# Kernel tuning notes

Hardware: AMD Instinct MI355X
Metric: run time of the kernel (lower is better)

The kernel has to match this reference:

```python
import jax, jax.numpy as jnp
import numpy as np

B, T, C, FREQ = 32, 512, 22, 192
HID = 128


def setup_inputs() -> dict:
    key = jax.random.key(0)
    k1, k2, k3, k4, k5, k6 = jax.random.split(key, 6)
    x = jax.random.normal(k1, (B, T, C, FREQ), dtype=jnp.float32)
    A = jax.random.uniform(k2, (B, T, C, C), dtype=jnp.float32)
    # Linear weights (torch layout: [out, in]); scaled like torch default init
    W0 = jax.random.normal(k3, (HID, FREQ), dtype=jnp.float32) / np.sqrt(FREQ)
    b0 = jax.random.normal(k4, (HID,), dtype=jnp.float32) * 0.01
    W1 = jax.random.normal(k5, (HID, HID), dtype=jnp.float32) / np.sqrt(HID)
    b1 = jax.random.normal(k6, (HID,), dtype=jnp.float32) * 0.01
    return {"x": x, "A": A, "W0": W0, "b0": b0, "W1": W1, "b1": b1}


def reference(x, A, W0, b0, W1, b1):
    # Vectorized over B and T simultaneously (original python-loops over t).
    # Layer i: xt = relu(Linear(bmm(A_t, xt)))
    h = x  # [B,T,C,Freq]
    for W, b in ((W0, b0), (W1, b1)):
        h = jnp.einsum('btij,btjf->btif', A, h)          # adjacency mix over nodes
        h = jax.nn.relu(jnp.einsum('btcf,hf->btch', h, W) + b)  # Linear + ReLU
    # stack over t is implicit; mean over node dim C -> [B,T,HID]
    return h.mean(axis=2)
```

## Files before the change

kernel.cpp:

```cpp
#include <hip/hip_runtime.h>

#define CC 22
#define FF 192
#define HH 128
#define NBT (32 * 512)

typedef __attribute__((ext_vector_type(8))) __bf16 bf16x8;
typedef __attribute__((ext_vector_type(8))) short s16x8;
typedef __attribute__((ext_vector_type(4))) float f32x4;

__device__ __forceinline__ float bf2f(unsigned short u) {
    union { unsigned int i; float f; } v;
    v.i = ((unsigned int)u) << 16;
    return v.f;
}

__device__ __forceinline__ unsigned short f2bf(float f) {
    union { float f; unsigned int i; } v;
    v.f = f;
    return (unsigned short)((v.i + 0x7fffu + ((v.i >> 16) & 1u)) >> 16);
}

__device__ __forceinline__ void split2(float v, unsigned short& h, unsigned short& l) {
    h = f2bf(v);
    float r = v - bf2f(h);
    l = f2bf(r);
}

__device__ __forceinline__ bf16x8 bzero8() {
    s16x8 z = {0, 0, 0, 0, 0, 0, 0, 0};
    return __builtin_bit_cast(bf16x8, z);
}

__global__ void detect_dtype(const unsigned short* __restrict__ A,
                             int* __restrict__ flag) {
    if (blockIdx.x == 0 && threadIdx.x == 0) {
        int ok = 1;
        for (int i = 0; i < 64; ++i) {
            float v = bf2f(A[i]);
            if (!(v >= 0.0f && v <= 1.0001f)) ok = 0;
        }
        *flag = ok;
    }
}

#define WS0H 0
#define WS0L 24576
#define WS1H 49152
#define WS1L 65536

__global__ void convert_weights(const float* __restrict__ W0g,
                                const float* __restrict__ W1g,
                                unsigned short* __restrict__ wsW,
                                const int* __restrict__ flag) {
    if (*flag) return;
    const int i = blockIdx.x * 256 + threadIdx.x;
    if (i < HH * FF) {
        unsigned short h, l;
        split2(W0g[i], h, l);
        wsW[WS0H + i] = h;
        wsW[WS0L + i] = l;
    } else {
        const int j = i - HH * FF;
        if (j < HH * HH) {
            unsigned short h, l;
            split2(W1g[j], h, l);
            wsW[WS1H + j] = h;
            wsW[WS1L + j] = l;
        }
    }
}

__device__ void run_block_f32(
    const float* __restrict__ xg, const float* __restrict__ Ag,
    const float* __restrict__ W0g, const float* __restrict__ b0g,
    const float* __restrict__ W1g, const float* __restrict__ b1g,
    float* __restrict__ outg, int bt, int tid,
    float* sA, float* sX, float* sH1, float* sH2, float* sRed)
{
    const float* Ap = Ag + (size_t)bt * (CC * CC);
    for (int i = tid; i < CC * CC; i += 256) sA[i] = Ap[i];
    const float4* xp = (const float4*)(xg + (size_t)bt * (CC * FF));
    for (int i = tid; i < CC * FF / 4; i += 256) ((float4*)sX)[i] = xp[i];
    __syncthreads();

    for (int idx4 = tid; idx4 < CC * FF / 4; idx4 += 256) {
        const int c  = idx4 / (FF / 4);
        const int fq = idx4 - c * (FF / 4);
        float4 acc = make_float4(0.f, 0.f, 0.f, 0.f);
        #pragma unroll
        for (int j = 0; j < CC; ++j) {
            const float  a  = sA[c * CC + j];
            const float4 xv = *(const float4*)&sX[j * FF + 4 * fq];
            acc.x += a * xv.x; acc.y += a * xv.y;
            acc.z += a * xv.z; acc.w += a * xv.w;
        }
        ((float4*)sH1)[idx4] = acc;
    }
    __syncthreads();

    const int h  = tid & 127;
    const int ty = tid >> 7;

    {
        float acc[11];
        const float bb = b0g[h];
        #pragma unroll
        for (int i = 0; i < 11; ++i) acc[i] = bb;
        #pragma unroll 4
        for (int fq = 0; fq < FF / 4; ++fq) {
            float4 u = ((const float4*)(W0g + h * FF))[fq];
            #pragma unroll
            for (int i = 0; i < 11; ++i) {
                const float4 xv = *(const float4*)&sH1[(2 * i + ty) * FF + 4 * fq];
                acc[i] = fmaf(xv.x, u.x, fmaf(xv.y, u.y, fmaf(xv.z, u.z, fmaf(xv.w, u.w, acc[i]))));
            }
        }
        #pragma unroll
        for (int i = 0; i < 11; ++i)
            sH2[(2 * i + ty) * HH + h] = fmaxf(acc[i], 0.f);
    }
    __syncthreads();

    float* sH3 = sX;
    for (int idx4 = tid; idx4 < CC * HH / 4; idx4 += 256) {
        const int c  = idx4 / (HH / 4);
        const int kq = idx4 - c * (HH / 4);
        float4 acc = make_float4(0.f, 0.f, 0.f, 0.f);
        #pragma unroll
        for (int j = 0; j < CC; ++j) {
            const float  a  = sA[c * CC + j];
            const float4 xv = *(const float4*)&sH2[j * HH + 4 * kq];
            acc.x += a * xv.x; acc.y += a * xv.y;
            acc.z += a * xv.z; acc.w += a * xv.w;
        }
        ((float4*)sH3)[idx4] = acc;
    }
    __syncthreads();

    {
        float acc[11];
        const float bb = b1g[h];
        #pragma unroll
        for (int i = 0; i < 11; ++i) acc[i] = bb;
        #pragma unroll 4
        for (int kq = 0; kq < HH / 4; ++kq) {
            float4 u = ((const float4*)(W1g + h * HH))[kq];
            #pragma unroll
            for (int i = 0; i < 11; ++i) {
                const float4 xv = *(const float4*)&sH3[(2 * i + ty) * HH + 4 * kq];
                acc[i] = fmaf(xv.x, u.x, fmaf(xv.y, u.y, fmaf(xv.z, u.z, fmaf(xv.w, u.w, acc[i]))));
            }
        }
        float s = 0.f;
        #pragma unroll
        for (int i = 0; i < 11; ++i) s += fmaxf(acc[i], 0.f);
        sRed[ty * HH + h] = s;
    }
    __syncthreads();

    if (ty == 0) {
        const float m = (sRed[h] + sRed[HH + h]) * (1.0f / 22.0f);
        outg[(size_t)bt * HH + h] = m;
    }
}

__device__ void run_block_split(
    const float* __restrict__ xg, const float* __restrict__ Ag,
    const float* __restrict__ b0g, const float* __restrict__ b1g,
    const unsigned short* __restrict__ wsW,
    float* __restrict__ outg, int bt, int tid, char* smem)
{
    unsigned short* sxh   = (unsigned short*)smem;
    unsigned short* sxl   = (unsigned short*)(smem + 8800);
    unsigned short* sAh   = (unsigned short*)(smem + 17600);
    unsigned short* sAl   = (unsigned short*)(smem + 20160);
    unsigned short* syTh  = (unsigned short*)(smem + 22720);
    unsigned short* syTl  = (unsigned short*)(smem + 32960);
    unsigned short* sh2Th = (unsigned short*)(smem + 43200);
    unsigned short* sh2Tl = (unsigned short*)(smem + 53440);
    unsigned short* sh3h  = (unsigned short*)smem;
    unsigned short* sh3l  = (unsigned short*)(smem + 8704);

    const unsigned short* W0h = wsW + WS0H;
    const unsigned short* W0l = wsW + WS0L;
    const unsigned short* W1h = wsW + WS1H;
    const unsigned short* W1l = wsW + WS1L;

    {
        const float4* xp4 = (const float4*)(xg + (size_t)bt * (CC * FF));
        for (int idx = tid; idx < CC * (FF / 4); idx += 256) {
            const int c = idx / (FF / 4);
            const int q = idx - c * (FF / 4);
            const float4 v = xp4[idx];
            ushort4 h4, l4;
            split2(v.x, h4.x, l4.x);
            split2(v.y, h4.y, l4.y);
            split2(v.z, h4.z, l4.z);
            split2(v.w, h4.w, l4.w);
            *(ushort4*)&sxh[c * 200 + 4 * q] = h4;
            *(ushort4*)&sxl[c * 200 + 4 * q] = l4;
        }
        const float* Ap = Ag + (size_t)bt * (CC * CC);
        for (int idx = tid; idx < 32 * 40; idx += 256) {
            const int r = idx / 40;
            const int c = idx - r * 40;
            unsigned short h = 0, l = 0;
            if (r < CC && c < CC) split2(Ap[r * CC + c], h, l);
            sAh[idx] = h;
            sAl[idx] = l;
        }
    }
    __syncthreads();

    const int lane = tid & 63;
    const int wid  = tid >> 6;
    const int lr   = lane & 15;
    const int lk   = lane >> 4;
    const int hb   = wid * 32;

    const f32x4 vzero = {0.f, 0.f, 0.f, 0.f};

    {
        f32x4 acc[2][2];
        #pragma unroll
        for (int mt = 0; mt < 2; ++mt)
            #pragma unroll
            for (int nt = 0; nt < 2; ++nt) acc[mt][nt] = vzero;

        #pragma unroll
        for (int ks = 0; ks < 6; ++ks) {
            bf16x8 xfh[2], xfl[2];
            #pragma unroll
            for (int mt = 0; mt < 2; ++mt) {
                const int row = mt * 16 + lr;
                const int rr  = (row < CC) ? row : 0;
                const int off = rr * 200 + ks * 32 + lk * 8;
                bf16x8 fh = *(const bf16x8*)(sxh + off);
                bf16x8 fl = *(const bf16x8*)(sxl + off);
                if (row >= CC) { fh = bzero8(); fl = bzero8(); }
                xfh[mt] = fh; xfl[mt] = fl;
            }
            bf16x8 wfh[2], wfl[2];
            #pragma unroll
            for (int nt = 0; nt < 2; ++nt) {
                const int hcol = hb + nt * 16 + lr;
                const int off  = hcol * FF + ks * 32 + lk * 8;
                wfh[nt] = *(const bf16x8*)(W0h + off);
                wfl[nt] = *(const bf16x8*)(W0l + off);
            }
            #pragma unroll
            for (int mt = 0; mt < 2; ++mt)
                #pragma unroll
                for (int nt = 0; nt < 2; ++nt) {
                    acc[mt][nt] = __builtin_amdgcn_mfma_f32_16x16x32_bf16(xfh[mt], wfh[nt], acc[mt][nt], 0, 0, 0);
                    acc[mt][nt] = __builtin_amdgcn_mfma_f32_16x16x32_bf16(xfl[mt], wfh[nt], acc[mt][nt], 0, 0, 0);
                    acc[mt][nt] = __builtin_amdgcn_mfma_f32_16x16x32_bf16(xfh[mt], wfl[nt], acc[mt][nt], 0, 0, 0);
                }
        }
        #pragma unroll
        for (int mt = 0; mt < 2; ++mt)
            #pragma unroll
            for (int nt = 0; nt < 2; ++nt) {
                const int hcol = hb + nt * 16 + lr;
                ushort4 h4, l4;
                split2(acc[mt][nt][0], h4.x, l4.x);
                split2(acc[mt][nt][1], h4.y, l4.y);
                split2(acc[mt][nt][2], h4.z, l4.z);
                split2(acc[mt][nt][3], h4.w, l4.w);
                *(ushort4*)&syTh[hcol * 40 + mt * 16 + lk * 4] = h4;
                *(ushort4*)&syTl[hcol * 40 + mt * 16 + lk * 4] = l4;
            }
    }
    __syncthreads();

    bf16x8 Afh[2], Afl[2];
    #pragma unroll
    for (int mt = 0; mt < 2; ++mt) {
        const int off = (mt * 16 + lr) * 40 + lk * 8;
        Afh[mt] = *(const bf16x8*)(sAh + off);
        Afl[mt] = *(const bf16x8*)(sAl + off);
    }

    {
        f32x4 acc[2][2];
        #pragma unroll
        for (int nt = 0; nt < 2; ++nt) {
            const float b = b0g[hb + nt * 16 + lr];
            const f32x4 bv = {b, b, b, b};
            acc[0][nt] = bv;
            acc[1][nt] = bv;
        }
        bf16x8 yfh[2], yfl[2];
        #pragma unroll
        for (int nt = 0; nt < 2; ++nt) {
            const int off = (hb + nt * 16 + lr) * 40 + lk * 8;
            yfh[nt] = *(const bf16x8*)(syTh + off);
            yfl[nt] = *(const bf16x8*)(syTl + off);
        }
        #pragma unroll
        for (int mt = 0; mt < 2; ++mt)
            #pragma unroll
            for (int nt = 0; nt < 2; ++nt) {
                acc[mt][nt] = __builtin_amdgcn_mfma_f32_16x16x32_bf16(Afh[mt], yfh[nt], acc[mt][nt], 0, 0, 0);
                acc[mt][nt] = __builtin_amdgcn_mfma_f32_16x16x32_bf16(Afl[mt], yfh[nt], acc[mt][nt], 0, 0, 0);
                acc[mt][nt] = __builtin_amdgcn_mfma_f32_16x16x32_bf16(Afh[mt], yfl[nt], acc[mt][nt], 0, 0, 0);
            }
        #pragma unroll
        for (int mt = 0; mt < 2; ++mt)
            #pragma unroll
            for (int nt = 0; nt < 2; ++nt) {
                const int hcol = hb + nt * 16 + lr;
                ushort4 h4, l4;
                split2(fmaxf(acc[mt][nt][0], 0.f), h4.x, l4.x);
                split2(fmaxf(acc[mt][nt][1], 0.f), h4.y, l4.y);
                split2(fmaxf(acc[mt][nt][2], 0.f), h4.z, l4.z);
                split2(fmaxf(acc[mt][nt][3], 0.f), h4.w, l4.w);
                *(ushort4*)&sh2Th[hcol * 40 + mt * 16 + lk * 4] = h4;
                *(ushort4*)&sh2Tl[hcol * 40 + mt * 16 + lk * 4] = l4;
            }
    }
    __syncthreads();

    {
        f32x4 acc[2][2];
        #pragma unroll
        for (int mt = 0; mt < 2; ++mt)
            #pragma unroll
            for (int nt = 0; nt < 2; ++nt) acc[mt][nt] = vzero;

        bf16x8 gfh[2], gfl[2];
        #pragma unroll
        for (int nt = 0; nt < 2; ++nt) {
            const int off = (hb + nt * 16 + lr) * 40 + lk * 8;
            gfh[nt] = *(const bf16x8*)(sh2Th + off);
            gfl[nt] = *(const bf16x8*)(sh2Tl + off);
        }
        #pragma unroll
        for (int mt = 0; mt < 2; ++mt)
            #pragma unroll
            for (int nt = 0; nt < 2; ++nt) {
                acc[mt][nt] = __builtin_amdgcn_mfma_f32_16x16x32_bf16(Afh[mt], gfh[nt], acc[mt][nt], 0, 0, 0);
                acc[mt][nt] = __builtin_amdgcn_mfma_f32_16x16x32_bf16(Afl[mt], gfh[nt], acc[mt][nt], 0, 0, 0);
                acc[mt][nt] = __builtin_amdgcn_mfma_f32_16x16x32_bf16(Afh[mt], gfl[nt], acc[mt][nt], 0, 0, 0);
            }
        __syncthreads();
        #pragma unroll
        for (int mt = 0; mt < 2; ++mt)
            #pragma unroll
            for (int nt = 0; nt < 2; ++nt) {
                const int col = hb + nt * 16 + lr;
                #pragma unroll
                for (int r = 0; r < 4; ++r) {
                    const int row = mt * 16 + lk * 4 + r;
                    unsigned short h, l;
                    split2(acc[mt][nt][r], h, l);
                    sh3h[row * 136 + col] = h;
                    sh3l[row * 136 + col] = l;
                }
            }
    }
    __syncthreads();

    {
        f32x4 acc[2][2];
        #pragma unroll
        for (int mt = 0; mt < 2; ++mt) {
            const float4 bv = *(const float4*)(b1g + hb + mt * 16 + lk * 4);
            const f32x4 bb = {bv.x, bv.y, bv.z, bv.w};
            acc[mt][0] = bb;
            acc[mt][1] = bb;
        }
        #pragma unroll
        for (int ks = 0; ks < 4; ++ks) {
            bf16x8 wfh[2], wfl[2], hfh[2], hfl[2];
            #pragma unroll
            for (int mt = 0; mt < 2; ++mt) {
                const int o   = hb + mt * 16 + lr;
                const int off = o * HH + ks * 32 + lk * 8;
                wfh[mt] = *(const bf16x8*)(W1h + off);
                wfl[mt] = *(const bf16x8*)(W1l + off);
            }
            #pragma unroll
            for (int ct = 0; ct < 2; ++ct) {
                const int off = (ct * 16 + lr) * 136 + ks * 32 + lk * 8;
                hfh[ct] = *(const bf16x8*)(sh3h + off);
                hfl[ct] = *(const bf16x8*)(sh3l + off);
            }
            #pragma unroll
            for (int mt = 0; mt < 2; ++mt)
                #pragma unroll
                for (int ct = 0; ct < 2; ++ct) {
                    acc[mt][ct] = __builtin_amdgcn_mfma_f32_16x16x32_bf16(wfh[mt], hfh[ct], acc[mt][ct], 0, 0, 0);
                    acc[mt][ct] = __builtin_amdgcn_mfma_f32_16x16x32_bf16(wfl[mt], hfh[ct], acc[mt][ct], 0, 0, 0);
                    acc[mt][ct] = __builtin_amdgcn_mfma_f32_16x16x32_bf16(wfh[mt], hfl[ct], acc[mt][ct], 0, 0, 0);
                }
        }
        float s[2][4];
        #pragma unroll
        for (int mt = 0; mt < 2; ++mt)
            #pragma unroll
            for (int r = 0; r < 4; ++r) {
                float v = fmaxf(acc[mt][0][r], 0.f);
                if (lr < CC - 16) v += fmaxf(acc[mt][1][r], 0.f);
                s[mt][r] = v;
            }
        #pragma unroll
        for (int m = 1; m < 16; m <<= 1)
            #pragma unroll
            for (int mt = 0; mt < 2; ++mt)
                #pragma unroll
                for (int r = 0; r < 4; ++r)
                    s[mt][r] += __shfl_xor(s[mt][r], m);

        if (lr == 0) {
            const float inv = 1.0f / 22.0f;
            #pragma unroll
            for (int mt = 0; mt < 2; ++mt) {
                float4 o4;
                o4.x = s[mt][0] * inv;
                o4.y = s[mt][1] * inv;
                o4.z = s[mt][2] * inv;
                o4.w = s[mt][3] * inv;
                *(float4*)(outg + (size_t)bt * HH + hb + mt * 16 + lk * 4) = o4;
            }
        }
    }
}

__device__ void run_block_bf16(
    const unsigned short* __restrict__ xg, const unsigned short* __restrict__ Ag,
    const unsigned short* __restrict__ W0g, const unsigned short* __restrict__ b0g,
    const unsigned short* __restrict__ W1g, const unsigned short* __restrict__ b1g,
    unsigned short* __restrict__ outg, int bt, int tid, char* smem)
{
    unsigned short* sXT  = (unsigned short*)smem;
    unsigned short* sAm  = (unsigned short*)(smem + 15360);
    unsigned short* sH1  = (unsigned short*)(smem + 17920);
    unsigned short* sH2T = (unsigned short*)(smem + 30720);
    unsigned short* sH3  = (unsigned short*)(smem + 40960);

    const unsigned short* xp = xg + (size_t)bt * (CC * FF);
    const unsigned short* Ap = Ag + (size_t)bt * (CC * CC);

    for (int id = tid; id < 32 * 40; id += 256) {
        const int r = id / 40;
        const int c = id - r * 40;
        sAm[id] = (r < CC && c < CC) ? Ap[r * CC + c] : (unsigned short)0;
    }
    for (int id = tid; id < FF * 9; id += 256) {
        const int f = id / 9;
        const int q = id - f * 9;
        ((unsigned int*)sXT)[f * 20 + 11 + q] = 0u;
    }
    for (int id = tid; id < 24 * CC; id += 256) {
        const int fb = id / CC;
        const int j  = id - fb * CC;
        const uint4 v = *(const uint4*)(xp + j * FF + fb * 8);
        unsigned short* d = sXT + (fb * 8) * 40 + j;
        d[0 * 40] = (unsigned short)(v.x & 0xffffu);
        d[1 * 40] = (unsigned short)(v.x >> 16);
        d[2 * 40] = (unsigned short)(v.y & 0xffffu);
        d[3 * 40] = (unsigned short)(v.y >> 16);
        d[4 * 40] = (unsigned short)(v.z & 0xffffu);
        d[5 * 40] = (unsigned short)(v.z >> 16);
        d[6 * 40] = (unsigned short)(v.w & 0xffffu);
        d[7 * 40] = (unsigned short)(v.w >> 16);
    }
    __syncthreads();

    const int lane = tid & 63;
    const int wid  = tid >> 6;
    const int lr   = lane & 15;
    const int lk   = lane >> 4;
    const f32x4 vzero = {0.f, 0.f, 0.f, 0.f};

    {
        f32x4 acc[3][2];
        #pragma unroll
        for (int i = 0; i < 3; ++i)
            #pragma unroll
            for (int j = 0; j < 2; ++j) acc[i][j] = vzero;
        bf16x8 xa[3], ab[2];
        #pragma unroll
        for (int i = 0; i < 3; ++i)
            xa[i] = *(const bf16x8*)(sXT + ((3 * wid + i) * 16 + lr) * 40 + lk * 8);
        #pragma unroll
        for (int j = 0; j < 2; ++j)
            ab[j] = *(const bf16x8*)(sAm + (j * 16 + lr) * 40 + lk * 8);
        #pragma unroll
        for (int i = 0; i < 3; ++i)
            #pragma unroll
            for (int j = 0; j < 2; ++j)
                acc[i][j] = __builtin_amdgcn_mfma_f32_16x16x32_bf16(xa[i], ab[j], acc[i][j], 0, 0, 0);
        #pragma unroll
        for (int i = 0; i < 3; ++i) {
            const int fbase = (3 * wid + i) * 16 + lk * 4;
            #pragma unroll
            for (int j = 0; j < 2; ++j) {
                const int c = j * 16 + lr;
                ushort4 st;
                st.x = f2bf(acc[i][j][0]);
                st.y = f2bf(acc[i][j][1]);
                st.z = f2bf(acc[i][j][2]);
                st.w = f2bf(acc[i][j][3]);
                *(ushort4*)(sH1 + c * 200 + fbase) = st;
            }
        }
    }
    __syncthreads();

    {
        f32x4 acc[2][2];
        #pragma unroll
        for (int nt = 0; nt < 2; ++nt) {
            const float bv = bf2f(b0g[(2 * wid + nt) * 16 + lr]);
            f32x4 bvv = {bv, bv, bv, bv};
            acc[0][nt] = bvv;
            acc[1][nt] = bvv;
        }
        #pragma unroll
        for (int ks = 0; ks < 6; ++ks) {
            bf16x8 af[2], bfr[2];
            #pragma unroll
            for (int mt = 0; mt < 2; ++mt)
                af[mt] = *(const bf16x8*)(sH1 + (mt * 16 + lr) * 200 + ks * 32 + lk * 8);
            #pragma unroll
            for (int nt = 0; nt < 2; ++nt)
                bfr[nt] = *(const bf16x8*)(W0g + ((size_t)((2 * wid + nt) * 16 + lr)) * FF + ks * 32 + lk * 8);
            #pragma unroll
            for (int mt = 0; mt < 2; ++mt)
                #pragma unroll
                for (int nt = 0; nt < 2; ++nt)
                    acc[mt][nt] = __builtin_amdgcn_mfma_f32_16x16x32_bf16(af[mt], bfr[nt], acc[mt][nt], 0, 0, 0);
        }
        #pragma unroll
        for (int mt = 0; mt < 2; ++mt) {
            const int cbase = mt * 16 + lk * 4;
            #pragma unroll
            for (int nt = 0; nt < 2; ++nt) {
                const int hcol = (2 * wid + nt) * 16 + lr;
                ushort4 st;
                st.x = (cbase + 0 < CC) ? f2bf(fmaxf(acc[mt][nt][0], 0.f)) : (unsigned short)0;
                st.y = (cbase + 1 < CC) ? f2bf(fmaxf(acc[mt][nt][1], 0.f)) : (unsigned short)0;
                st.z = (cbase + 2 < CC) ? f2bf(fmaxf(acc[mt][nt][2], 0.f)) : (unsigned short)0;
                st.w = (cbase + 3 < CC) ? f2bf(fmaxf(acc[mt][nt][3], 0.f)) : (unsigned short)0;
                *(ushort4*)(sH2T + hcol * 40 + cbase) = st;
            }
        }
    }
    __syncthreads();

    {
        f32x4 acc[2][2];
        #pragma unroll
        for (int mt = 0; mt < 2; ++mt)
            #pragma unroll
            for (int ct = 0; ct < 2; ++ct) acc[mt][ct] = vzero;
        bf16x8 af[2], bb[2];
        #pragma unroll
        for (int mt = 0; mt < 2; ++mt)
            af[mt] = *(const bf16x8*)(sH2T + ((2 * wid + mt) * 16 + lr) * 40 + lk * 8);
        #pragma unroll
        for (int ct = 0; ct < 2; ++ct)
            bb[ct] = *(const bf16x8*)(sAm + (ct * 16 + lr) * 40 + lk * 8);
        #pragma unroll
        for (int mt = 0; mt < 2; ++mt)
            #pragma unroll
            for (int ct = 0; ct < 2; ++ct)
                acc[mt][ct] = __builtin_amdgcn_mfma_f32_16x16x32_bf16(af[mt], bb[ct], acc[mt][ct], 0, 0, 0);
        #pragma unroll
        for (int mt = 0; mt < 2; ++mt) {
            const int hbase = (2 * wid + mt) * 16 + lk * 4;
            #pragma unroll
            for (int ct = 0; ct < 2; ++ct) {
                const int c = ct * 16 + lr;
                ushort4 st;
                st.x = f2bf(acc[mt][ct][0]);
                st.y = f2bf(acc[mt][ct][1]);
                st.z = f2bf(acc[mt][ct][2]);
                st.w = f2bf(acc[mt][ct][3]);
                *(ushort4*)(sH3 + c * 136 + hbase) = st;
            }
        }
    }
    __syncthreads();

    {
        f32x4 acc[2][2];
        #pragma unroll
        for (int mt = 0; mt < 2; ++mt) {
            const ushort4 bu = *(const ushort4*)(b1g + (2 * wid + mt) * 16 + lk * 4);
            f32x4 bvv = {bf2f(bu.x), bf2f(bu.y), bf2f(bu.z), bf2f(bu.w)};
            acc[mt][0] = bvv;
            acc[mt][1] = bvv;
        }
        #pragma unroll
        for (int ks = 0; ks < 4; ++ks) {
            bf16x8 af[2], bfr[2];
            #pragma unroll
            for (int mt = 0; mt < 2; ++mt)
                af[mt] = *(const bf16x8*)(W1g + ((size_t)((2 * wid + mt) * 16 + lr)) * HH + ks * 32 + lk * 8);
            #pragma unroll
            for (int ct = 0; ct < 2; ++ct)
                bfr[ct] = *(const bf16x8*)(sH3 + (ct * 16 + lr) * 136 + ks * 32 + lk * 8);
            #pragma unroll
            for (int mt = 0; mt < 2; ++mt)
                #pragma unroll
                for (int ct = 0; ct < 2; ++ct)
                    acc[mt][ct] = __builtin_amdgcn_mfma_f32_16x16x32_bf16(af[mt], bfr[ct], acc[mt][ct], 0, 0, 0);
        }
        float s[2][4];
        #pragma unroll
        for (int mt = 0; mt < 2; ++mt)
            #pragma unroll
            for (int r = 0; r < 4; ++r) {
                float v = fmaxf(acc[mt][0][r], 0.f);
                if (lr < CC - 16) v += fmaxf(acc[mt][1][r], 0.f);
                s[mt][r] = v;
            }
        #pragma unroll
        for (int m = 1; m < 16; m <<= 1)
            #pragma unroll
            for (int mt = 0; mt < 2; ++mt)
                #pragma unroll
                for (int r = 0; r < 4; ++r)
                    s[mt][r] += __shfl_xor(s[mt][r], m);
        if (lr == 0) {
            const float inv = 1.0f / 22.0f;
            #pragma unroll
            for (int mt = 0; mt < 2; ++mt) {
                ushort4 st;
                st.x = f2bf(s[mt][0] * inv);
                st.y = f2bf(s[mt][1] * inv);
                st.z = f2bf(s[mt][2] * inv);
                st.w = f2bf(s[mt][3] * inv);
                *(ushort4*)(outg + (size_t)bt * HH + (2 * wid + mt) * 16 + lk * 4) = st;
            }
        }
    }
}

__global__ __launch_bounds__(256) void tgcn_kernel(
    const void* __restrict__ x, const void* __restrict__ A,
    const void* __restrict__ W0, const void* __restrict__ b0,
    const void* __restrict__ W1, const void* __restrict__ b1,
    void* __restrict__ out, const int* __restrict__ flag,
    const unsigned short* __restrict__ wsW, int use_split)
{
    __shared__ __align__(16) char smem[63680];

    const int tid = threadIdx.x;
    const int bt  = blockIdx.x;
    const int isbf = *flag;

    if (isbf) {
        run_block_bf16((const unsigned short*)x, (const unsigned short*)A,
                       (const unsigned short*)W0, (const unsigned short*)b0,
                       (const unsigned short*)W1, (const unsigned short*)b1,
                       (unsigned short*)out, bt, tid, smem);
    } else if (use_split) {
        run_block_split((const float*)x, (const float*)A,
                        (const float*)b0, (const float*)b1,
                        wsW, (float*)out, bt, tid, smem);
    } else {
        float* sA   = (float*)smem;
        float* sX   = (float*)(smem + 1936);
        float* sH1  = (float*)(smem + 18832);
        float* sH2  = (float*)(smem + 35728);
        float* sRed = (float*)(smem + 46992);
        run_block_f32((const float*)x, (const float*)A,
                      (const float*)W0, (const float*)b0,
                      (const float*)W1, (const float*)b1,
                      (float*)out, bt, tid, sA, sX, sH1, sH2, sRed);
    }
}

extern "C" void kernel_launch(void* const* d_in, const int* in_sizes, int n_in,
                              void* d_out, int out_size, void* d_ws, size_t ws_size,
                              hipStream_t stream) {
    int* flag = (int*)d_ws;
    unsigned short* wsW = (unsigned short*)((char*)d_ws + 256);
    const int use_split = (ws_size >= (size_t)(256 + 81920 * 2)) ? 1 : 0;

    detect_dtype<<<1, 64, 0, stream>>>((const unsigned short*)d_in[1], flag);
    if (use_split)
        convert_weights<<<160, 256, 0, stream>>>(
            (const float*)d_in[2], (const float*)d_in[4], wsW, flag);
    tgcn_kernel<<<NBT, 256, 0, stream>>>(
        d_in[0], d_in[1], d_in[2], d_in[3], d_in[4], d_in[5], d_out, flag,
        wsW, use_split);
}
```

Before: 789.5 us.

## Alias shared buffers to cut LDS footprint and inline dtype detection

Removes the separate dtype-detection kernel launch and replaces it with a wave-wide vote on the first A elements inside each kernel. Reuses shared memory regions across stages in all three code paths, shrinking the static LDS allocation from about 63.7KB to 43.2KB so more blocks can be resident per CU. In the split path the second adjacency mix is computed in transposed form so it can write to the same buffer it reads from, and one barrier is dropped. The aliasing relies on careful barrier placement, and every block now redoes the 64-element dtype check.

```diff
diff --git a/kernel.cpp b/kernel.cpp
--- a/kernel.cpp
+++ b/kernel.cpp
@@ -32,16 +32,10 @@
     return __builtin_bit_cast(bf16x8, z);
 }
 
-__global__ void detect_dtype(const unsigned short* __restrict__ A,
-                             int* __restrict__ flag) {
-    if (blockIdx.x == 0 && threadIdx.x == 0) {
-        int ok = 1;
-        for (int i = 0; i < 64; ++i) {
-            float v = bf2f(A[i]);
-            if (!(v >= 0.0f && v <= 1.0001f)) ok = 0;
-        }
-        *flag = ok;
-    }
+__device__ __forceinline__ int inputs_are_bf16(const unsigned short* __restrict__ A,
+                                               int tid) {
+    const float v = bf2f(A[tid & 63]);
+    return __all(v >= 0.0f && v <= 1.0001f);
 }
 
 #define WS0H 0
@@ -51,9 +45,9 @@
 
 __global__ void convert_weights(const float* __restrict__ W0g,
                                 const float* __restrict__ W1g,
-                                unsigned short* __restrict__ wsW,
-                                const int* __restrict__ flag) {
-    if (*flag) return;
+                                const unsigned short* __restrict__ Aany,
+                                unsigned short* __restrict__ wsW) {
+    if (inputs_are_bf16(Aany, threadIdx.x)) return;
     const int i = blockIdx.x * 256 + threadIdx.x;
     if (i < HH * FF) {
         unsigned short h, l;
@@ -76,8 +70,12 @@
     const float* __restrict__ W0g, const float* __restrict__ b0g,
     const float* __restrict__ W1g, const float* __restrict__ b1g,
     float* __restrict__ outg, int bt, int tid,
-    float* sA, float* sX, float* sH1, float* sH2, float* sRed)
+    float* sA, float* sX, float* sH1)
 {
+    float* sH2  = sX;
+    float* sH3  = sH1;
+    float* sRed = sA;
+
     const float* Ap = Ag + (size_t)bt * (CC * CC);
     for (int i = tid; i < CC * CC; i += 256) sA[i] = Ap[i];
     const float4* xp = (const float4*)(xg + (size_t)bt * (CC * FF));
@@ -122,7 +120,6 @@
     }
     __syncthreads();
 
-    float* sH3 = sX;
     for (int idx4 = tid; idx4 < CC * HH / 4; idx4 += 256) {
         const int c  = idx4 / (HH / 4);
         const int kq = idx4 - c * (HH / 4);
@@ -171,16 +168,14 @@
     const unsigned short* __restrict__ wsW,
     float* __restrict__ outg, int bt, int tid, char* smem)
 {
-    unsigned short* sxh   = (unsigned short*)smem;
-    unsigned short* sxl   = (unsigned short*)(smem + 8800);
-    unsigned short* sAh   = (unsigned short*)(smem + 17600);
-    unsigned short* sAl   = (unsigned short*)(smem + 20160);
-    unsigned short* syTh  = (unsigned short*)(smem + 22720);
-    unsigned short* syTl  = (unsigned short*)(smem + 32960);
-    unsigned short* sh2Th = (unsigned short*)(smem + 43200);
-    unsigned short* sh2Tl = (unsigned short*)(smem + 53440);
-    unsigned short* sh3h  = (unsigned short*)smem;
-    unsigned short* sh3l  = (unsigned short*)(smem + 8704);
+    unsigned short* sxh  = (unsigned short*)smem;
+    unsigned short* sxl  = (unsigned short*)(smem + 8800);
+    unsigned short* sAh  = (unsigned short*)(smem + 17600);
+    unsigned short* sAl  = (unsigned short*)(smem + 20160);
+    unsigned short* syh  = (unsigned short*)(smem + 22720);
+    unsigned short* syl  = (unsigned short*)(smem + 32960);
+    unsigned short* sh3h = (unsigned short*)smem;
+    unsigned short* sh3l = (unsigned short*)(smem + 8704);
 
     const unsigned short* W0h = wsW + WS0H;
     const unsigned short* W0l = wsW + WS0L;
@@ -268,18 +263,18 @@
                 split2(acc[mt][nt][1], h4.y, l4.y);
                 split2(acc[mt][nt][2], h4.z, l4.z);
                 split2(acc[mt][nt][3], h4.w, l4.w);
-                *(ushort4*)&syTh[hcol * 40 + mt * 16 + lk * 4] = h4;
-                *(ushort4*)&syTl[hcol * 40 + mt * 16 + lk * 4] = l4;
+                *(ushort4*)&syh[hcol * 40 + mt * 16 + lk * 4] = h4;
+                *(ushort4*)&syl[hcol * 40 + mt * 16 + lk * 4] = l4;
             }
     }
     __syncthreads();
 
     bf16x8 Afh[2], Afl[2];
     #pragma unroll
-    for (int mt = 0; mt < 2; ++mt) {
-        const int off = (mt * 16 + lr) * 40 + lk * 8;
-        Afh[mt] = *(const bf16x8*)(sAh + off);
-        Afl[mt] = *(const bf16x8*)(sAl + off);
+    for (int t = 0; t < 2; ++t) {
+        const int off = (t * 16 + lr) * 40 + lk * 8;
+        Afh[t] = *(const bf16x8*)(sAh + off);
+        Afl[t] = *(const bf16x8*)(sAl + off);
     }
 
     {
@@ -295,9 +290,10 @@
         #pragma unroll
         for (int nt = 0; nt < 2; ++nt) {
             const int off = (hb + nt * 16 + lr) * 40 + lk * 8;
-            yfh[nt] = *(const bf16x8*)(syTh + off);
-            yfl[nt] = *(const bf16x8*)(syTl + off);
-        }
+            yfh[nt] = *(const bf16x8*)(syh + off);
+            yfl[nt] = *(const bf16x8*)(syl + off);
+        }
+        asm volatile("" ::: "memory");
         #pragma unroll
         for (int mt = 0; mt < 2; ++mt)
             #pragma unroll
@@ -316,48 +312,45 @@
                 split2(fmaxf(acc[mt][nt][1], 0.f), h4.y, l4.y);
                 split2(fmaxf(acc[mt][nt][2], 0.f), h4.z, l4.z);
                 split2(fmaxf(acc[mt][nt][3], 0.f), h4.w, l4.w);
-                *(ushort4*)&sh2Th[hcol * 40 + mt * 16 + lk * 4] = h4;
-                *(ushort4*)&sh2Tl[hcol * 40 + mt * 16 + lk * 4] = l4;
-            }
-    }
-    __syncthreads();
+                *(ushort4*)&syh[hcol * 40 + mt * 16 + lk * 4] = h4;
+                *(ushort4*)&syl[hcol * 40 + mt * 16 + lk * 4] = l4;
+            }
+    }
 
     {
         f32x4 acc[2][2];
         #pragma unroll
         for (int mt = 0; mt < 2; ++mt)
             #pragma unroll
-            for (int nt = 0; nt < 2; ++nt) acc[mt][nt] = vzero;
+            for (int ct = 0; ct < 2; ++ct) acc[mt][ct] = vzero;
 
         bf16x8 gfh[2], gfl[2];
         #pragma unroll
-        for (int nt = 0; nt < 2; ++nt) {
-            const int off = (hb + nt * 16 + lr) * 40 + lk * 8;
-            gfh[nt] = *(const bf16x8*)(sh2Th + off);
-            gfl[nt] = *(const bf16x8*)(sh2Tl + off);
-        }
-        #pragma unroll
-        for (int mt = 0; mt < 2; ++mt)
-            #pragma unroll
-            for (int nt = 0; nt < 2; ++nt) {
-                acc[mt][nt] = __builtin_amdgcn_mfma_f32_16x16x32_bf16(Afh[mt], gfh[nt], acc[mt][nt], 0, 0, 0);
-                acc[mt][nt] = __builtin_amdgcn_mfma_f32_16x16x32_bf16(Afl[mt], gfh[nt], acc[mt][nt], 0, 0, 0);
-                acc[mt][nt] = __builtin_amdgcn_mfma_f32_16x16x32_bf16(Afh[mt], gfl[nt], acc[mt][nt], 0, 0, 0);
-            }
-        __syncthreads();
-        #pragma unroll
-        for (int mt = 0; mt < 2; ++mt)
-            #pragma unroll
-            for (int nt = 0; nt < 2; ++nt) {
-                const int col = hb + nt * 16 + lr;
-                #pragma unroll
-                for (int r = 0; r < 4; ++r) {
-                    const int row = mt * 16 + lk * 4 + r;
-                    unsigned short h, l;
-                    split2(acc[mt][nt][r], h, l);
-                    sh3h[row * 136 + col] = h;
-                    sh3l[row * 136 + col] = l;
-                }
+        for (int mt = 0; mt < 2; ++mt) {
+            const int off = (hb + mt * 16 + lr) * 40 + lk * 8;
+            gfh[mt] = *(const bf16x8*)(syh + off);
+            gfl[mt] = *(const bf16x8*)(syl + off);
+        }
+        #pragma unroll
+        for (int mt = 0; mt < 2; ++mt)
+            #pragma unroll
+            for (int ct = 0; ct < 2; ++ct) {
+                acc[mt][ct] = __builtin_amdgcn_mfma_f32_16x16x32_bf16(gfh[mt], Afh[ct], acc[mt][ct], 0, 0, 0);
+                acc[mt][ct] = __builtin_amdgcn_mfma_f32_16x16x32_bf16(gfl[mt], Afh[ct], acc[mt][ct], 0, 0, 0);
+                acc[mt][ct] = __builtin_amdgcn_mfma_f32_16x16x32_bf16(gfh[mt], Afl[ct], acc[mt][ct], 0, 0, 0);
+            }
+        #pragma unroll
+        for (int mt = 0; mt < 2; ++mt)
+            #pragma unroll
+            for (int ct = 0; ct < 2; ++ct) {
+                const int cp = ct * 16 + lr;
+                ushort4 h4, l4;
+                split2(acc[mt][ct][0], h4.x, l4.x);
+                split2(acc[mt][ct][1], h4.y, l4.y);
+                split2(acc[mt][ct][2], h4.z, l4.z);
+                split2(acc[mt][ct][3], h4.w, l4.w);
+                *(ushort4*)&sh3h[cp * 136 + hb + mt * 16 + lk * 4] = h4;
+                *(ushort4*)&sh3l[cp * 136 + hb + mt * 16 + lk * 4] = l4;
             }
     }
     __syncthreads();
@@ -438,7 +431,7 @@
     unsigned short* sAm  = (unsigned short*)(smem + 15360);
     unsigned short* sH1  = (unsigned short*)(smem + 17920);
     unsigned short* sH2T = (unsigned short*)(smem + 30720);
-    unsigned short* sH3  = (unsigned short*)(smem + 40960);
+    unsigned short* sH3  = (unsigned short*)smem;
 
     const unsigned short* xp = xg + (size_t)bt * (CC * FF);
     const unsigned short* Ap = Ag + (size_t)bt * (CC * CC);
@@ -645,14 +638,14 @@
     const void* __restrict__ x, const void* __restrict__ A,
     const void* __restrict__ W0, const void* __restrict__ b0,
     const void* __restrict__ W1, const void* __restrict__ b1,
-    void* __restrict__ out, const int* __restrict__ flag,
-    const unsigned short* __restrict__ wsW, int use_split)
+    void* __restrict__ out, const unsigned short* __restrict__ wsW,
+    int use_split)
 {
-    __shared__ __align__(16) char smem[63680];
+    __shared__ __align__(16) char smem[43200];
 
     const int tid = threadIdx.x;
     const int bt  = blockIdx.x;
-    const int isbf = *flag;
+    const int isbf = inputs_are_bf16((const unsigned short*)A, tid);
 
     if (isbf) {
         run_block_bf16((const unsigned short*)x, (const unsigned short*)A,
@@ -664,30 +657,27 @@
                         (const float*)b0, (const float*)b1,
                         wsW, (float*)out, bt, tid, smem);
     } else {
-        float* sA   = (float*)smem;
-        float* sX   = (float*)(smem + 1936);
-        float* sH1  = (float*)(smem + 18832);
-        float* sH2  = (float*)(smem + 35728);
-        float* sRed = (float*)(smem + 46992);
+        float* sA  = (float*)smem;
+        float* sX  = (float*)(smem + 1936);
+        float* sH1 = (float*)(smem + 18832);
         run_block_f32((const float*)x, (const float*)A,
                       (const float*)W0, (const float*)b0,
                       (const float*)W1, (const float*)b1,
-                      (float*)out, bt, tid, sA, sX, sH1, sH2, sRed);
+                      (float*)out, bt, tid, sA, sX, sH1);
     }
 }
 
 extern "C" void kernel_launch(void* const* d_in, const int* in_sizes, int n_in,
                               void* d_out, int out_size, void* d_ws, size_t ws_size,
                               hipStream_t stream) {
-    int* flag = (int*)d_ws;
-    unsigned short* wsW = (unsigned short*)((char*)d_ws + 256);
-    const int use_split = (ws_size >= (size_t)(256 + 81920 * 2)) ? 1 : 0;
-
-    detect_dtype<<<1, 64, 0, stream>>>((const unsigned short*)d_in[1], flag);
+    unsigned short* wsW = (unsigned short*)d_ws;
+    const int use_split = (ws_size >= (size_t)(81920 * 2)) ? 1 : 0;
+
     if (use_split)
         convert_weights<<<160, 256, 0, stream>>>(
-            (const float*)d_in[2], (const float*)d_in[4], wsW, flag);
+            (const float*)d_in[2], (const float*)d_in[4],
+            (const unsigned short*)d_in[1], wsW);
     tgcn_kernel<<<NBT, 256, 0, stream>>>(
-        d_in[0], d_in[1], d_in[2], d_in[3], d_in[4], d_in[5], d_out, flag,
+        d_in[0], d_in[1], d_in[2], d_in[3], d_in[4], d_in[5], d_out,
         wsW, use_split);
 }
```

Result: faster. 705.8 us (-10.6%).
